# Kernel optimization log

Measured on AMD Instinct MI355X. Metric: run time of the kernel, lower is better.

The kernel has to match this reference:

```python
import jax, jax.numpy as jnp
import numpy as np

B, F0, D = 2048, 39, 16
CROSS = [200, 200, 200]


def setup_inputs() -> dict:
    key = jax.random.key(0)
    ks = jax.random.split(key, 7)
    inp = {"x": jax.random.normal(ks[0], (B, F0, D), dtype=jnp.float32)}
    prev = F0
    for i, c in enumerate(CROSS):
        # Conv1d(in=F0*prev, out=c, kernel=1) weight reshaped to (c, F0, prev)
        scale = 1.0 / np.sqrt(F0 * prev)
        inp[f"W{i}"] = jax.random.normal(ks[1 + 2 * i], (c, F0, prev), dtype=jnp.float32) * scale
        inp[f"b{i}"] = jnp.zeros((c,), dtype=jnp.float32)
        prev = c
    return inp


def reference(x, W0, b0, W1, b1, W2, b2):
    # x: (B, F0, D). Each CIN layer in torch materializes x0*h -> (B, F0*prev, D)
    # then applies a kernel-1 Conv1d. Mathematically this is the bilinear
    # contraction below (same values, no quadratic intermediate).
    x0 = x
    h = x
    xs = []
    for W, b in ((W0, b0), (W1, b1), (W2, b2)):
        # z[b,o,d] = sum_{f,g} W[o,f,g] * x0[b,f,d] * h[b,g,d] + bias[o]
        z = jnp.einsum('bfd,bgd,ofg->bod', x0, h, W) + b[None, :, None]
        h = jax.nn.relu(z)
        xs.append(h)
    # concat over channel dim, sum-pool over embed dim -> (B, sum(cross_sizes))
    return jnp.sum(jnp.concatenate(xs, axis=1), axis=2)
```

## Files before the change

### kernel.cpp

```cpp
#include <hip/hip_runtime.h>
#include <hip/hip_bf16.h>
#include <stdint.h>

typedef __attribute__((ext_vector_type(8))) short bf16x8;
typedef __attribute__((ext_vector_type(4))) float f32x4;
typedef unsigned short u16;
typedef unsigned int u32;

#define GLL(gp, lp) __builtin_amdgcn_global_load_lds( \
    (const __attribute__((address_space(1))) void*)(gp), \
    (__attribute__((address_space(3))) void*)(lp), 16, 0, 0)

__device__ __forceinline__ u16 f2bf_rne(float v) {
    u32 u = __float_as_uint(v);
    u32 r = (u + 0x7fffu + ((u >> 16) & 1u)) >> 16;
    return (u16)r;
}


__global__ void pack_x_kernel(const float* __restrict__ x, u16* __restrict__ xbd) {
    int idx = blockIdx.x * 256 + threadIdx.x;
    if (idx >= 32768 * 40) return;
    int m = idx / 40, f = idx - m * 40;
    int b = m >> 4, d = m & 15;
    float v = (f < 39) ? x[(b * 39 + f) * 16 + d] : 0.0f;
    xbd[idx] = f2bf_rne(v);
}

__global__ void pack_w0_kernel(const float* __restrict__ W, u16* __restrict__ Wp) {
    int idx = blockIdx.x * 256 + threadIdx.x;
    if (idx >= 224 * 1792) return;
    int o = idx / 1792, k = idx - o * 1792;
    int f = k / 40, g = k - f * 40;
    float v = (o < 200 && f < 39 && g < 39) ? W[(o * 39 + f) * 39 + g] : 0.0f;
    Wp[idx] = f2bf_rne(v);
}

__global__ void pack_w12_kernel(const float* __restrict__ W, u16* __restrict__ Wp) {
    int idx = blockIdx.x * 256 + threadIdx.x;
    if (idx >= 224 * 8192) return;
    int o = idx / 8192, k = idx - o * 8192;
    int f = k / 208, g = k - f * 208;
    float v = (o < 200 && f < 39 && g < 200) ? W[o * 7800 + f * 200 + g] : 0.0f;
    Wp[idx] = f2bf_rne(v);
}

template <int LAYER>
__global__ __launch_bounds__(512, 2) void cin_gemm4(
    const u16* __restrict__ Xbd,
    const u16* __restrict__ Hglb,
    const u16* __restrict__ Wp,
    const float* __restrict__ bias,
    u16* __restrict__ Hout,
    float* __restrict__ out)
{
    constexpr int KP     = (LAYER == 0) ? 1792 : 8192;
    constexpr int NGROUP = KP / 256;
    constexpr u32 MAGIC  = (LAYER == 0) ? 3277u : 10083u;
    constexpr int SHIFT  = (LAYER == 0) ? 17 : 21;
    constexpr int GS     = (LAYER == 0) ? 40 : 208;
    constexpr int HROW   = (LAYER == 0) ? 40 : 208;
    constexpr int WOFF   = 20480;
    constexpr int WBUF   = 57344;

    __shared__ __align__(16) char smem[WOFF + 2 * WBUF];
    u16* Xl = (u16*)smem;

    const int bid  = blockIdx.x;
    const int mblk = bid >> 1, nblk = bid & 1;
    const int m0    = mblk * 256;
    const int ncol0 = nblk * 112;
    const int NT    = nblk ? 6 : 7;
    const int tid  = threadIdx.x;
    const int lane = tid & 63, wid = tid >> 6;
    const int mg = wid & 3, kg = wid >> 2;
    const int rowl = lane & 15, grp = lane >> 4;

    {
        const char* xsrc = (const char*)(Xbd + (size_t)m0 * 40);
        for (int i = wid; i < 20; i += 8)
            GLL(xsrc + i * 1024 + lane * 16, smem + i * 1024);
    }
    const size_t wlsrc = (size_t)(ncol0 + (lane >> 2)) * KP + wid * 32 + (lane & 3) * 8;
    {
        char* wb = smem + WOFF + wid * 7168;
        #pragma unroll
        for (int j = 0; j < 7; ++j)
            GLL((const char*)(Wp + wlsrc + (size_t)j * 16 * KP), wb + j * 1024);
    }

    int xro[4];
    size_t hrg[4];
    #pragma unroll
    for (int s = 0; s < 4; ++s) {
        int r = mg * 64 + s * 16 + rowl;
        xro[s] = r * 40;
        hrg[s] = (size_t)(m0 + r) * HROW;
    }

    f32x4 acc[4][7];
    #pragma unroll
    for (int s = 0; s < 4; ++s)
        #pragma unroll
        for (int t = 0; t < 7; ++t) {
            f32x4 z = {0.f, 0.f, 0.f, 0.f};
            acc[s][t] = z;
        }

    for (int g = 0; g < NGROUP; ++g) {
        __syncthreads();
        if (g + 1 < NGROUP) {
            char* wb = smem + WOFF + ((g + 1) & 1) * WBUF + wid * 7168;
            const u16* gsrc = Wp + wlsrc + (size_t)(g + 1) * 256;
            #pragma unroll
            for (int j = 0; j < 7; ++j)
                GLL((const char*)(gsrc + (size_t)j * 16 * KP), wb + j * 1024);
        }
        const u16* wbase = (const u16*)(smem + WOFF + (g & 1) * WBUF);
        #pragma unroll
        for (int p = 0; p < 4; ++p) {
            int k0 = g * 256 + p * 64 + kg * 32 + grp * 8;
            u32 f = ((u32)k0 * MAGIC) >> SHIFT;
            f = (f > 39u) ? 39u : f;
            int g0 = k0 - (int)f * GS;
            bf16x8 afrag[4];
            #pragma unroll
            for (int s = 0; s < 4; ++s) {
                u16 xs = Xl[xro[s] + (int)f];
                bf16x8 hv = *(const bf16x8*)(Hglb + hrg[s] + g0);
                float xf = __uint_as_float(((u32)xs) << 16);
                union { bf16x8 v; u32 w[4]; } hu, au;
                hu.v = hv;
                #pragma unroll
                for (int j = 0; j < 4; ++j) {
                    float lo = __uint_as_float(hu.w[j] << 16);
                    float hi = __uint_as_float(hu.w[j] & 0xffff0000u);
                    float pl = xf * lo;
                    float ph = xf * hi;
                    u32 pk;
                    asm("v_cvt_pk_bf16_f32 %0, %1, %2" : "=v"(pk) : "v"(pl), "v"(ph));
                    au.w[j] = pk;
                }
                afrag[s] = au.v;
            }
            const u16* wbR = wbase + (p * 2 + kg) * 3584 + rowl * 32 + grp * 8;
            #pragma unroll
            for (int t = 0; t < 7; ++t) {
                if (t < NT) {
                    bf16x8 bfrag = *(const bf16x8*)&wbR[t * 512];
                    #pragma unroll
                    for (int s = 0; s < 4; ++s)
                        acc[s][t] = __builtin_amdgcn_mfma_f32_16x16x32_bf16(afrag[s], bfrag, acc[s][t], 0, 0, 0);
                }
            }
        }
    }

    __syncthreads();
    float* red = (float*)smem;
    const int rbase = mg * 7168 + lane * 4;
    if (kg == 1) {
        #pragma unroll
        for (int s = 0; s < 4; ++s)
            #pragma unroll
            for (int t = 0; t < 7; ++t)
                if (t < NT)
                    *(f32x4*)&red[rbase + (s * 7 + t) * 256] = acc[s][t];
    }
    __syncthreads();

    if (kg == 0) {
        float bias_t[7];
        #pragma unroll
        for (int t = 0; t < 7; ++t) {
            int oc = ncol0 + t * 16 + rowl;
            bias_t[t] = (t < NT && oc < 200) ? bias[oc] : 0.0f;
        }
        #pragma unroll
        for (int s = 0; s < 4; ++s) {
            int mrow0 = m0 + mg * 64 + s * 16;
            int bidx = mrow0 >> 4;
            #pragma unroll
            for (int t = 0; t < 7; ++t) {
                if (t < NT) {
                    int oc = ncol0 + t * 16 + rowl;
                    f32x4 o = *(const f32x4*)&red[rbase + (s * 7 + t) * 256];
                    f32x4 v = acc[s][t];
                    float h0 = fmaxf(v[0] + o[0] + bias_t[t], 0.0f);
                    float h1 = fmaxf(v[1] + o[1] + bias_t[t], 0.0f);
                    float h2 = fmaxf(v[2] + o[2] + bias_t[t], 0.0f);
                    float h3 = fmaxf(v[3] + o[3] + bias_t[t], 0.0f);
                    if constexpr (LAYER < 2) {
                        size_t rb = (size_t)(mrow0 + grp * 4) * 208 + oc;
                        Hout[rb]           = f2bf_rne(h0);
                        Hout[rb + 208]     = f2bf_rne(h1);
                        Hout[rb + 2*208]   = f2bf_rne(h2);
                        Hout[rb + 3*208]   = f2bf_rne(h3);
                    }
                    float ssum = (h0 + h1) + (h2 + h3);
                    ssum += __shfl_xor(ssum, 16);
                    ssum += __shfl_xor(ssum, 32);
                    if (grp == 0 && oc < 200)
                        out[(size_t)bidx * 600 + LAYER * 200 + oc] = ssum;
                }
            }
        }
    }
}

extern "C" void kernel_launch(void* const* d_in, const int* in_sizes, int n_in,
                              void* d_out, int out_size, void* d_ws, size_t ws_size,
                              hipStream_t stream) {
    const float* x  = (const float*)d_in[0];
    const float* W0 = (const float*)d_in[1];
    const float* b0 = (const float*)d_in[2];
    const float* W1 = (const float*)d_in[3];
    const float* b1 = (const float*)d_in[4];
    const float* W2 = (const float*)d_in[5];
    const float* b2 = (const float*)d_in[6];
    float* out = (float*)d_out;

    char* ws = (char*)d_ws;
    u16* xbd = (u16*)(ws);
    u16* wp0 = (u16*)(ws + 2622464);
    u16* wp1 = (u16*)(ws + 3425280);
    u16* wp2 = (u16*)(ws + 7095296);
    u16* h1  = (u16*)(ws + 10765312);
    u16* h2  = (u16*)(ws + 24397824);

    pack_x_kernel<<<5120, 256, 0, stream>>>(x, xbd);
    pack_w0_kernel<<<1568, 256, 0, stream>>>(W0, wp0);
    pack_w12_kernel<<<7168, 256, 0, stream>>>(W1, wp1);
    pack_w12_kernel<<<7168, 256, 0, stream>>>(W2, wp2);

    cin_gemm4<0><<<256, 512, 0, stream>>>(xbd, xbd, wp0, b0, h1, out);
    cin_gemm4<1><<<256, 512, 0, stream>>>(xbd, h1, wp1, b1, h2, out);
    cin_gemm4<2><<<256, 512, 0, stream>>>(xbd, h2, wp2, b2, (u16*)nullptr, out);
}
```

Before: 342.4 us.

## Stage H tile in LDS and load W fragments directly into registers

The CIN GEMM kernel now copies the block's full H tile (256 rows × 208 bf16) into shared memory once, instead of reading H from global memory on every k-step. The W operand is no longer staged through double-buffered LDS with per-group barriers. Each wave instead loads its B fragments straight from global memory into registers, using a two-deep register ping-pong. This removes the per-iteration __syncthreads and the LDS traffic for W, but makes W loads uncoalesced 16-byte strided reads with latency that is only hidden by one step of register prefetch. Shared memory use grows to about 127KB for layers 1 and 2, and a clamp on g0 is added to keep reads inside the staged rows.

```diff
diff --git a/kernel.cpp b/kernel.cpp
--- a/kernel.cpp
+++ b/kernel.cpp
@@ -46,25 +46,28 @@
 }
 
 template <int LAYER>
-__global__ __launch_bounds__(512, 2) void cin_gemm4(
+__global__ __launch_bounds__(512, 2) void cin_gemm5(
     const u16* __restrict__ Xbd,
-    const u16* __restrict__ Hglb,
+    const u16* __restrict__ Hin,
     const u16* __restrict__ Wp,
     const float* __restrict__ bias,
     u16* __restrict__ Hout,
     float* __restrict__ out)
 {
-    constexpr int KP     = (LAYER == 0) ? 1792 : 8192;
-    constexpr int NGROUP = KP / 256;
-    constexpr u32 MAGIC  = (LAYER == 0) ? 3277u : 10083u;
-    constexpr int SHIFT  = (LAYER == 0) ? 17 : 21;
-    constexpr int GS     = (LAYER == 0) ? 40 : 208;
-    constexpr int HROW   = (LAYER == 0) ? 40 : 208;
-    constexpr int WOFF   = 20480;
-    constexpr int WBUF   = 57344;
-
-    __shared__ __align__(16) char smem[WOFF + 2 * WBUF];
+    constexpr int KP    = (LAYER == 0) ? 1792 : 8192;
+    constexpr int NPAIR = KP / 64;
+    constexpr u32 MAGIC = (LAYER == 0) ? 3277u : 10083u;
+    constexpr int SHIFT = (LAYER == 0) ? 17 : 21;
+    constexpr int GS    = (LAYER == 0) ? 40 : 208;
+    constexpr int GCL   = (LAYER == 0) ? 32 : 200;
+    constexpr int HROW  = (LAYER == 0) ? 40 : 208;
+    constexpr int HSZ   = (LAYER == 0) ? 0 : 106496;
+    constexpr int SMEMA = 20480 + HSZ;
+    constexpr int SMEM  = (SMEMA > 114688) ? SMEMA : 114688;
+
+    __shared__ __align__(16) char smem[SMEM];
     u16* Xl = (u16*)smem;
+    u16* Hl = (u16*)(smem + 20480);
 
     const int bid  = blockIdx.x;
     const int mblk = bid >> 1, nblk = bid & 1;
@@ -81,22 +84,20 @@
         for (int i = wid; i < 20; i += 8)
             GLL(xsrc + i * 1024 + lane * 16, smem + i * 1024);
     }
-    const size_t wlsrc = (size_t)(ncol0 + (lane >> 2)) * KP + wid * 32 + (lane & 3) * 8;
-    {
-        char* wb = smem + WOFF + wid * 7168;
-        #pragma unroll
-        for (int j = 0; j < 7; ++j)
-            GLL((const char*)(Wp + wlsrc + (size_t)j * 16 * KP), wb + j * 1024);
-    }
-
-    int xro[4];
-    size_t hrg[4];
+    if constexpr (LAYER > 0) {
+        const char* hsrc = (const char*)(Hin + (size_t)m0 * 208);
+        for (int i = wid; i < 104; i += 8)
+            GLL(hsrc + i * 1024 + lane * 16, smem + 20480 + i * 1024);
+    }
+
+    int xro[4], hro[4];
     #pragma unroll
     for (int s = 0; s < 4; ++s) {
         int r = mg * 64 + s * 16 + rowl;
         xro[s] = r * 40;
-        hrg[s] = (size_t)(m0 + r) * HROW;
-    }
+        hro[s] = r * HROW;
+    }
+    const u16* Hb = (LAYER == 0) ? Xl : Hl;
 
     f32x4 acc[4][7];
     #pragma unroll
@@ -107,54 +108,58 @@
             acc[s][t] = z;
         }
 
-    for (int g = 0; g < NGROUP; ++g) {
-        __syncthreads();
-        if (g + 1 < NGROUP) {
-            char* wb = smem + WOFF + ((g + 1) & 1) * WBUF + wid * 7168;
-            const u16* gsrc = Wp + wlsrc + (size_t)(g + 1) * 256;
-            #pragma unroll
-            for (int j = 0; j < 7; ++j)
-                GLL((const char*)(gsrc + (size_t)j * 16 * KP), wb + j * 1024);
-        }
-        const u16* wbase = (const u16*)(smem + WOFF + (g & 1) * WBUF);
-        #pragma unroll
-        for (int p = 0; p < 4; ++p) {
-            int k0 = g * 256 + p * 64 + kg * 32 + grp * 8;
-            u32 f = ((u32)k0 * MAGIC) >> SHIFT;
-            f = (f > 39u) ? 39u : f;
-            int g0 = k0 - (int)f * GS;
-            bf16x8 afrag[4];
-            #pragma unroll
-            for (int s = 0; s < 4; ++s) {
-                u16 xs = Xl[xro[s] + (int)f];
-                bf16x8 hv = *(const bf16x8*)(Hglb + hrg[s] + g0);
-                float xf = __uint_as_float(((u32)xs) << 16);
-                union { bf16x8 v; u32 w[4]; } hu, au;
-                hu.v = hv;
-                #pragma unroll
-                for (int j = 0; j < 4; ++j) {
-                    float lo = __uint_as_float(hu.w[j] << 16);
-                    float hi = __uint_as_float(hu.w[j] & 0xffff0000u);
-                    float pl = xf * lo;
-                    float ph = xf * hi;
-                    u32 pk;
-                    asm("v_cvt_pk_bf16_f32 %0, %1, %2" : "=v"(pk) : "v"(pl), "v"(ph));
-                    au.w[j] = pk;
-                }
-                afrag[s] = au.v;
-            }
-            const u16* wbR = wbase + (p * 2 + kg) * 3584 + rowl * 32 + grp * 8;
-            #pragma unroll
-            for (int t = 0; t < 7; ++t) {
-                if (t < NT) {
-                    bf16x8 bfrag = *(const bf16x8*)&wbR[t * 512];
-                    #pragma unroll
-                    for (int s = 0; s < 4; ++s)
-                        acc[s][t] = __builtin_amdgcn_mfma_f32_16x16x32_bf16(afrag[s], bfrag, acc[s][t], 0, 0, 0);
-                }
-            }
-        }
-    }
+    const u16* WbBase = Wp + (size_t)(ncol0 + rowl) * KP + kg * 32 + grp * 8;
+
+    bf16x8 bA[7], bB[7];
+
+#define LOADB(koff, dst) { \
+    _Pragma("unroll") \
+    for (int t = 0; t < 7; ++t) \
+        dst[t] = *(const bf16x8*)(WbBase + (size_t)t * 16 * KP + (koff)); }
+
+#define COMPUTE(pr, bR) { \
+    int k0 = (pr) * 64 + kg * 32 + grp * 8; \
+    u32 f = ((u32)k0 * MAGIC) >> SHIFT; \
+    f = (f > 39u) ? 39u : f; \
+    int g0 = k0 - (int)f * GS; \
+    g0 = (g0 > GCL) ? GCL : g0; \
+    bf16x8 afrag[4]; \
+    _Pragma("unroll") \
+    for (int s = 0; s < 4; ++s) { \
+        u16 xs = Xl[xro[s] + (int)f]; \
+        bf16x8 hv = *(const bf16x8*)&Hb[hro[s] + g0]; \
+        float xf = __uint_as_float(((u32)xs) << 16); \
+        union { bf16x8 v; u32 w[4]; } hu, au; \
+        hu.v = hv; \
+        _Pragma("unroll") \
+        for (int j = 0; j < 4; ++j) { \
+            float lo = __uint_as_float(hu.w[j] << 16); \
+            float hi = __uint_as_float(hu.w[j] & 0xffff0000u); \
+            float pl = xf * lo, ph2 = xf * hi; \
+            u32 pk; \
+            asm("v_cvt_pk_bf16_f32 %0, %1, %2" : "=v"(pk) : "v"(pl), "v"(ph2)); \
+            au.w[j] = pk; \
+        } \
+        afrag[s] = au.v; \
+    } \
+    _Pragma("unroll") \
+    for (int t = 0; t < 7; ++t) { \
+        _Pragma("unroll") \
+        for (int s = 0; s < 4; ++s) \
+            acc[s][t] = __builtin_amdgcn_mfma_f32_16x16x32_bf16(afrag[s], bR[t], acc[s][t], 0, 0, 0); \
+    } }
+
+    LOADB(0, bA);
+    __syncthreads();
+
+    for (int pr = 0; pr < NPAIR; pr += 2) {
+        LOADB((pr + 1) * 64, bB);
+        COMPUTE(pr, bA);
+        if (pr + 2 < NPAIR) LOADB((pr + 2) * 64, bA);
+        COMPUTE(pr + 1, bB);
+    }
+#undef LOADB
+#undef COMPUTE
 
     __syncthreads();
     float* red = (float*)smem;
@@ -233,7 +238,7 @@
     pack_w12_kernel<<<7168, 256, 0, stream>>>(W1, wp1);
     pack_w12_kernel<<<7168, 256, 0, stream>>>(W2, wp2);
 
-    cin_gemm4<0><<<256, 512, 0, stream>>>(xbd, xbd, wp0, b0, h1, out);
-    cin_gemm4<1><<<256, 512, 0, stream>>>(xbd, h1, wp1, b1, h2, out);
-    cin_gemm4<2><<<256, 512, 0, stream>>>(xbd, h2, wp2, b2, (u16*)nullptr, out);
-}
+    cin_gemm5<0><<<256, 512, 0, stream>>>(xbd, xbd, wp0, b0, h1, out);
+    cin_gemm5<1><<<256, 512, 0, stream>>>(xbd, h1, wp1, b1, h2, out);
+    cin_gemm5<2><<<256, 512, 0, stream>>>(xbd, h2, wp2, b2, (u16*)nullptr, out);
+}
```

Measured after the change: 489.9 us. 1.43x slower.
